# Kernel optimization log

Measured on AMD Instinct MI355X. Metric: run time of the kernel, lower is better.

Reference implementation:

```python
import jax, jax.numpy as jnp
import numpy as np

N_NODES = 100_000
N_EDGES = 3_200_000
IN_CH = 128
HID = 128


def setup_inputs() -> dict:
    key = jax.random.key(0)
    k1, k2, k3, k4, k5 = jax.random.split(key, 5)
    x = jax.random.normal(k1, (N_NODES, IN_CH), dtype=jnp.float32)
    edge_index = jax.random.randint(k2, (2, N_EDGES), 0, N_NODES, dtype=jnp.int64)
    # GCNConv params: glorot-style weights, zero bias (as in PyG defaults)
    s1 = 1.0 / np.sqrt(IN_CH)
    s2 = 1.0 / np.sqrt(HID)
    W1 = jax.random.uniform(k3, (IN_CH, HID), jnp.float32, -s1, s1)
    b1 = jnp.zeros((HID,), jnp.float32)
    W2 = jax.random.uniform(k4, (HID, HID), jnp.float32, -s2, s2)
    b2 = jnp.zeros((HID,), jnp.float32)
    return {"x": x, "edge_index": edge_index, "W1": W1, "b1": b1, "W2": W2, "b2": b2}


def _gcn_conv(x, src, dst, W, b):
    """PyG GCNConv: add self-loops, symmetric D^-1/2 (A+I) D^-1/2 norm,
    linear transform first, then aggregate, then bias."""
    n = x.shape[0]
    loops = jnp.arange(n, dtype=src.dtype)
    s = jnp.concatenate([src, loops])          # [E+N]
    d = jnp.concatenate([dst, loops])          # [E+N]
    w = jnp.ones(s.shape[0], dtype=x.dtype)    # edge_weight=None -> ones
    deg = jax.ops.segment_sum(w, d, num_segments=n)            # [N]
    dinv = jnp.where(deg > 0, jax.lax.rsqrt(deg), 0.0)         # deg^-1/2
    norm = dinv[s] * w * dinv[d]                                # [E+N]
    xw = x @ W                                                  # [N, H]
    msg = xw[s] * norm[:, None]                                 # [E+N, H] gather
    out = jax.ops.segment_sum(msg, d, num_segments=n)           # [N, H] scatter
    return out + b


def reference(x, edge_index, W1, b1, W2, b2):
    src, dst = edge_index[0], edge_index[1]
    h1 = jax.nn.relu(_gcn_conv(x, src, dst, W1, b1))
    h2 = jax.nn.relu(_gcn_conv(h1, src, dst, W2, b2))
    return jnp.concatenate([h1, h2], axis=1)   # [N, 2*HID]
```

## Files before the change

### kernel.cpp

```cpp
#include <hip/hip_runtime.h>
#include <hip/hip_bf16.h>
#include <stdint.h>

#define NN 100000
#define BSH 9
#define BSZ 512
#define NBUCK 196
#define CAP 24576

static __device__ __forceinline__ float bf_lo(unsigned int u) {
    union { unsigned int i; float f; } c; c.i = u << 16; return c.f;
}
static __device__ __forceinline__ float bf_hi(unsigned int u) {
    union { unsigned int i; float f; } c; c.i = u & 0xffff0000u; return c.f;
}
static __device__ __forceinline__ unsigned short f2bf(float f) {
    union { float f; unsigned int i; } c; c.f = f;
    unsigned int r = (c.i + 0x7fffu + ((c.i >> 16) & 1u)) >> 16;
    return (unsigned short)r;
}

__global__ void k_detect(const int* __restrict__ eb, int* __restrict__ flag) {
    int v = eb[2 * threadIdx.x + 1];
    unsigned long long m = __ballot(v == 0);
    if (threadIdx.x == 0) *flag = (m == ~0ull) ? 1 : 0;
}

__global__ void k_init(int* __restrict__ gcursor) {
    int i = threadIdx.x;
    if (i < NBUCK) gcursor[i] = i * CAP;
}

__global__ __launch_bounds__(256) void k_bucket(const int* __restrict__ eb, int E,
                                                const int* __restrict__ flag,
                                                int* __restrict__ gcursor,
                                                unsigned int* __restrict__ pairs) {
    __shared__ int hist[NBUCK];
    __shared__ int gbase[NBUCK];
    int t = threadIdx.x;
    int sh = *flag;
    size_t base = (size_t)blockIdx.x * 4096;
    for (int i = t; i < NBUCK; i += 256) hist[i] = 0;
    __syncthreads();
    int srcs[16], rank[16], bks[16], dls[16];
#pragma unroll
    for (int k = 0; k < 16; k++) {
        size_t e = base + (size_t)k * 256 + t;
        if (e < (size_t)E) {
            int s = eb[e << sh];
            int d = eb[((size_t)E + e) << sh];
            int b = d >> BSH;
            srcs[k] = s; bks[k] = b; dls[k] = d & (BSZ - 1);
            rank[k] = atomicAdd(&hist[b], 1);
        } else {
            bks[k] = -1;
        }
    }
    __syncthreads();
    for (int i = t; i < NBUCK; i += 256) {
        int c = hist[i];
        gbase[i] = (c > 0) ? atomicAdd(&gcursor[i], c) : 0;
    }
    __syncthreads();
#pragma unroll
    for (int k = 0; k < 16; k++) {
        if (bks[k] >= 0) {
            int pos = gbase[bks[k]] + rank[k];
            if (pos < (bks[k] + 1) * CAP)
                pairs[pos] = ((unsigned int)dls[k] << 17) | (unsigned int)srcs[k];
        }
    }
}

__global__ __launch_bounds__(256) void k_pass2(const unsigned int* __restrict__ pairs,
                                               const int* __restrict__ gcursor,
                                               int* __restrict__ csr, int* __restrict__ ptr,
                                               int* __restrict__ degv, float* __restrict__ dinv) {
    __shared__ int hist[BSZ];
    __shared__ int lofs[BSZ];
    __shared__ int cur[BSZ];
    __shared__ int scanw[256];
    __shared__ int lcsr[CAP];
    int b = blockIdx.x, t = threadIdx.x;
    int base = b * CAP;
    int cnt = gcursor[b] - base;
    if (cnt > CAP) cnt = CAP;
    for (int i = t; i < BSZ; i += 256) hist[i] = 0;
    __syncthreads();
    for (int i = t; i < cnt; i += 256) {
        unsigned int p = pairs[base + i];
        atomicAdd(&hist[p >> 17], 1);
    }
    __syncthreads();
    int a = hist[2 * t] + hist[2 * t + 1];
    scanw[t] = a;
    __syncthreads();
    for (int d = 1; d < 256; d <<= 1) {
        int x = (t >= d) ? scanw[t - d] : 0;
        __syncthreads();
        scanw[t] += x;
        __syncthreads();
    }
    int excl = scanw[t] - a;
    lofs[2 * t] = excl;
    lofs[2 * t + 1] = excl + hist[2 * t];
    cur[2 * t] = excl;
    cur[2 * t + 1] = excl + hist[2 * t];
    __syncthreads();
    for (int i = t; i < cnt; i += 256) {
        unsigned int p = pairs[base + i];
        int dl = p >> 17;
        int pos = atomicAdd(&cur[dl], 1);
        lcsr[pos] = (int)(p & 0x1FFFFu);
    }
    __syncthreads();
    for (int i = t; i < cnt; i += 256) csr[base + i] = lcsr[i];
    int n0 = b << BSH;
    for (int g = t; g < BSZ; g += 256) {
        int n = n0 + g;
        if (n < NN) {
            int dg = hist[g];
            degv[n] = dg;
            ptr[n] = base + lofs[g];
            dinv[n] = rsqrtf((float)(dg + 1));
        }
    }
}

__global__ __launch_bounds__(256) void k_gemm(const float* __restrict__ A, int lda,
                                              const float* __restrict__ W,
                                              unsigned short* __restrict__ outb, int M) {
    __shared__ float Wl[32 * 128];
    __shared__ float Al[64 * 33];
    int t = threadIdx.x;
    int row0 = blockIdx.x * 64;
    int cg = t & 15, rg = t >> 4;
    int c0 = cg * 8, r0 = rg * 4;
    float acc[4][8];
#pragma unroll
    for (int i = 0; i < 4; i++)
#pragma unroll
        for (int j = 0; j < 8; j++) acc[i][j] = 0.f;

    for (int kb = 0; kb < 4; kb++) {
        __syncthreads();
        const float4* Wg = (const float4*)(W + kb * 32 * 128);
        float4* Wl4 = (float4*)Wl;
#pragma unroll
        for (int i = 0; i < 4; i++) Wl4[t + 256 * i] = Wg[t + 256 * i];
#pragma unroll
        for (int i = 0; i < 2; i++) {
            int idx = t + 256 * i;
            int r = idx >> 3, c4 = idx & 7;
            int grow = row0 + r;
            float4 v = make_float4(0.f, 0.f, 0.f, 0.f);
            if (grow < M) v = *(const float4*)(A + (size_t)grow * lda + kb * 32 + c4 * 4);
            float* dp = &Al[r * 33 + c4 * 4];
            dp[0] = v.x; dp[1] = v.y; dp[2] = v.z; dp[3] = v.w;
        }
        __syncthreads();
#pragma unroll 8
        for (int k = 0; k < 32; k++) {
            float wv[8];
            *(float4*)&wv[0] = *(const float4*)&Wl[k * 128 + c0];
            *(float4*)&wv[4] = *(const float4*)&Wl[k * 128 + c0 + 4];
            float av[4];
#pragma unroll
            for (int i = 0; i < 4; i++) av[i] = Al[(r0 + i) * 33 + k];
#pragma unroll
            for (int i = 0; i < 4; i++)
#pragma unroll
                for (int j = 0; j < 8; j++)
                    acc[i][j] = fmaf(av[i], wv[j], acc[i][j]);
        }
    }
#pragma unroll
    for (int i = 0; i < 4; i++) {
        int grow = row0 + r0 + i;
        if (grow < M) {
            unsigned int w[4];
#pragma unroll
            for (int j = 0; j < 4; j++)
                w[j] = (unsigned int)f2bf(acc[i][2 * j]) | ((unsigned int)f2bf(acc[i][2 * j + 1]) << 16);
            uint4 pk = make_uint4(w[0], w[1], w[2], w[3]);
            *(uint4*)(outb + (size_t)grow * 128 + c0) = pk;
        }
    }
}

__global__ __launch_bounds__(256) void k_aggr(const unsigned short* __restrict__ xwb,
                                              const int* __restrict__ csr, const int* __restrict__ ptr,
                                              const int* __restrict__ degv,
                                              const float* __restrict__ dinv, const float* __restrict__ bias,
                                              float* __restrict__ outf, int N) {
    int wid = (blockIdx.x * 256 + threadIdx.x) >> 6;
    int lane = threadIdx.x & 63;
    if (wid >= N) return;
    int n = wid;
    int st = ptr[n];
    int en = st + degv[n];
    const unsigned short* xl = xwb + (lane << 1);
    float acc0 = 0.f, acc1 = 0.f;
    for (int j = st; j < en; j += 64) {
        int e = j + lane;
        int sp = (e < en) ? csr[e] : 0;
        float dp = (e < en) ? dinv[sp] : 0.f;
        int cnt = en - j; if (cnt > 64) cnt = 64;
        int cntr = (cnt + 3) & ~3;
        for (int q = 0; q < cntr; q += 4) {
            int s0 = __shfl(sp, q), s1 = __shfl(sp, q + 1);
            int s2 = __shfl(sp, q + 2), s3 = __shfl(sp, q + 3);
            float d0 = __shfl(dp, q), d1 = __shfl(dp, q + 1);
            float d2 = __shfl(dp, q + 2), d3 = __shfl(dp, q + 3);
            unsigned int u0 = *(const unsigned int*)(xl + ((size_t)s0 << 7));
            unsigned int u1 = *(const unsigned int*)(xl + ((size_t)s1 << 7));
            unsigned int u2 = *(const unsigned int*)(xl + ((size_t)s2 << 7));
            unsigned int u3 = *(const unsigned int*)(xl + ((size_t)s3 << 7));
            acc0 = fmaf(bf_lo(u0), d0, acc0); acc1 = fmaf(bf_hi(u0), d0, acc1);
            acc0 = fmaf(bf_lo(u1), d1, acc0); acc1 = fmaf(bf_hi(u1), d1, acc1);
            acc0 = fmaf(bf_lo(u2), d2, acc0); acc1 = fmaf(bf_hi(u2), d2, acc1);
            acc0 = fmaf(bf_lo(u3), d3, acc0); acc1 = fmaf(bf_hi(u3), d3, acc1);
        }
    }
    float dn = dinv[n];
    {
        unsigned int u = *(const unsigned int*)(xl + ((size_t)n << 7));
        acc0 = fmaf(bf_lo(u), dn, acc0);
        acc1 = fmaf(bf_hi(u), dn, acc1);
    }
    float o0 = fmaxf(fmaf(acc0, dn, bias[lane << 1]), 0.f);
    float o1 = fmaxf(fmaf(acc1, dn, bias[(lane << 1) + 1]), 0.f);
    *(float2*)(outf + (size_t)n * 256 + (lane << 1)) = make_float2(o0, o1);
}

extern "C" void kernel_launch(void* const* d_in, const int* in_sizes, int n_in,
                              void* d_out, int out_size, void* d_ws, size_t ws_size,
                              hipStream_t stream) {
    const float* x  = (const float*)d_in[0];
    const int*   eb = (const int*)d_in[1];
    const float* W1 = (const float*)d_in[2];
    const float* b1 = (const float*)d_in[3];
    const float* W2 = (const float*)d_in[4];
    const float* b2 = (const float*)d_in[5];
    float* out = (float*)d_out;

    int E = in_sizes[1] / 2;

    char* w = (char*)d_ws;
    size_t o = 0;
    auto carve = [&](size_t bytes) { char* p = w + o; o += (bytes + 255) & ~(size_t)255; return p; };
    int*   flag    = (int*)carve(4);
    int*   gcursor = (int*)carve((size_t)NBUCK * 4);
    int*   ptr     = (int*)carve((size_t)NN * 4);
    int*   deg     = (int*)carve((size_t)NN * 4);
    float* dinv    = (float*)carve((size_t)NN * 4);
    int*   csr     = (int*)carve((size_t)NBUCK * CAP * 4);
    size_t big = (size_t)NN * 128 * 2;
    size_t pb  = (size_t)NBUCK * CAP * 4;
    char* shared_region = carve(big > pb ? big : pb);
    unsigned int*   pairs = (unsigned int*)shared_region;
    unsigned short* xwb   = (unsigned short*)shared_region;
    (void)ws_size;

    int EB4 = (E + 4095) / 4096;
    int GB  = (NN + 63) / 64;
    int AB  = (NN + 3) / 4;

    k_detect<<<1, 64, 0, stream>>>(eb, flag);
    k_init<<<1, 256, 0, stream>>>(gcursor);
    k_bucket<<<EB4, 256, 0, stream>>>(eb, E, flag, gcursor, pairs);
    k_pass2<<<NBUCK, 256, 0, stream>>>(pairs, gcursor, csr, ptr, deg, dinv);

    k_gemm<<<GB, 256, 0, stream>>>(x, 128, W1, xwb, NN);
    k_aggr<<<AB, 256, 0, stream>>>(xwb, csr, ptr, deg, dinv, b1, out, NN);

    k_gemm<<<GB, 256, 0, stream>>>(out, 256, W2, xwb, NN);
    k_aggr<<<AB, 256, 0, stream>>>(xwb, csr, ptr, deg, dinv, b2, out + 128, NN);
}
```

Baseline: 538.4 us.

## Prescale GEMM output by dinv, sort neighbours by source, unroll gather by eight

The GEMM epilogue now multiplies each row by dinv[row] before the bf16 store. This removes the per-edge dinv gather and multiply from the aggregation loop, which becomes a plain sum unrolled by eight. Padding lanes point at a zeroed extra row NN that k_init clears. pass2 orders each node's neighbour list by the high bits of the source index to improve cache locality of the gathers. The separate detect kernel is folded into k_bucket. The costs are a larger shared-memory histogram in pass2, and bf16 rounding now happens after the dinv scaling.

```diff
diff --git a/kernel.cpp b/kernel.cpp
--- a/kernel.cpp
+++ b/kernel.cpp
@@ -20,28 +20,28 @@
     return (unsigned short)r;
 }
 
-__global__ void k_detect(const int* __restrict__ eb, int* __restrict__ flag) {
-    int v = eb[2 * threadIdx.x + 1];
-    unsigned long long m = __ballot(v == 0);
-    if (threadIdx.x == 0) *flag = (m == ~0ull) ? 1 : 0;
-}
-
-__global__ void k_init(int* __restrict__ gcursor) {
+__global__ void k_init(int* __restrict__ gcursor, unsigned int* __restrict__ xwb_row_nn) {
     int i = threadIdx.x;
     if (i < NBUCK) gcursor[i] = i * CAP;
+    if (i < 64) xwb_row_nn[i] = 0u;
 }
 
 __global__ __launch_bounds__(256) void k_bucket(const int* __restrict__ eb, int E,
-                                                const int* __restrict__ flag,
                                                 int* __restrict__ gcursor,
                                                 unsigned int* __restrict__ pairs) {
     __shared__ int hist[NBUCK];
     __shared__ int gbase[NBUCK];
+    __shared__ int shflag;
     int t = threadIdx.x;
-    int sh = *flag;
+    if (t < 64) {
+        int v = eb[2 * t + 1];
+        unsigned long long m = __ballot(v == 0);
+        if (t == 0) shflag = (m == ~0ull) ? 1 : 0;
+    }
+    for (int i = t; i < NBUCK; i += 256) hist[i] = 0;
+    __syncthreads();
+    int sh = shflag;
     size_t base = (size_t)blockIdx.x * 4096;
-    for (int i = t; i < NBUCK; i += 256) hist[i] = 0;
-    __syncthreads();
     int srcs[16], rank[16], bks[16], dls[16];
 #pragma unroll
     for (int k = 0; k < 16; k++) {
@@ -76,23 +76,30 @@
                                                const int* __restrict__ gcursor,
                                                int* __restrict__ csr, int* __restrict__ ptr,
                                                int* __restrict__ degv, float* __restrict__ dinv) {
+    __shared__ int hist2[BSZ * 8];
+    __shared__ int cur2[BSZ * 8];
     __shared__ int hist[BSZ];
     __shared__ int lofs[BSZ];
-    __shared__ int cur[BSZ];
     __shared__ int scanw[256];
     __shared__ int lcsr[CAP];
     int b = blockIdx.x, t = threadIdx.x;
     int base = b * CAP;
     int cnt = gcursor[b] - base;
     if (cnt > CAP) cnt = CAP;
-    for (int i = t; i < BSZ; i += 256) hist[i] = 0;
+    for (int i = t; i < BSZ * 8; i += 256) hist2[i] = 0;
     __syncthreads();
     for (int i = t; i < cnt; i += 256) {
         unsigned int p = pairs[base + i];
-        atomicAdd(&hist[p >> 17], 1);
-    }
-    __syncthreads();
-    int a = hist[2 * t] + hist[2 * t + 1];
+        int key = (int)((p >> 17) << 3) | (int)((p & 0x1FFFFu) >> 14);
+        atomicAdd(&hist2[key], 1);
+    }
+    __syncthreads();
+    int dl0 = 2 * t, dl1 = 2 * t + 1;
+    int h0 = 0, h1 = 0;
+#pragma unroll
+    for (int oc = 0; oc < 8; oc++) { h0 += hist2[(dl0 << 3) | oc]; h1 += hist2[(dl1 << 3) | oc]; }
+    hist[dl0] = h0; hist[dl1] = h1;
+    int a = h0 + h1;
     scanw[t] = a;
     __syncthreads();
     for (int d = 1; d < 256; d <<= 1) {
@@ -102,16 +109,20 @@
         __syncthreads();
     }
     int excl = scanw[t] - a;
-    lofs[2 * t] = excl;
-    lofs[2 * t + 1] = excl + hist[2 * t];
-    cur[2 * t] = excl;
-    cur[2 * t + 1] = excl + hist[2 * t];
+    lofs[dl0] = excl;
+    lofs[dl1] = excl + h0;
+    int run = excl;
+#pragma unroll
+    for (int oc = 0; oc < 8; oc++) { cur2[(dl0 << 3) | oc] = run; run += hist2[(dl0 << 3) | oc]; }
+#pragma unroll
+    for (int oc = 0; oc < 8; oc++) { cur2[(dl1 << 3) | oc] = run; run += hist2[(dl1 << 3) | oc]; }
     __syncthreads();
     for (int i = t; i < cnt; i += 256) {
         unsigned int p = pairs[base + i];
-        int dl = p >> 17;
-        int pos = atomicAdd(&cur[dl], 1);
-        lcsr[pos] = (int)(p & 0x1FFFFu);
+        int src = (int)(p & 0x1FFFFu);
+        int key = (int)((p >> 17) << 3) | (src >> 14);
+        int pos = atomicAdd(&cur2[key], 1);
+        lcsr[pos] = src;
     }
     __syncthreads();
     for (int i = t; i < cnt; i += 256) csr[base + i] = lcsr[i];
@@ -129,6 +140,7 @@
 
 __global__ __launch_bounds__(256) void k_gemm(const float* __restrict__ A, int lda,
                                               const float* __restrict__ W,
+                                              const float* __restrict__ dinv,
                                               unsigned short* __restrict__ outb, int M) {
     __shared__ float Wl[32 * 128];
     __shared__ float Al[64 * 33];
@@ -178,10 +190,12 @@
     for (int i = 0; i < 4; i++) {
         int grow = row0 + r0 + i;
         if (grow < M) {
+            float dv = dinv[grow];
             unsigned int w[4];
 #pragma unroll
             for (int j = 0; j < 4; j++)
-                w[j] = (unsigned int)f2bf(acc[i][2 * j]) | ((unsigned int)f2bf(acc[i][2 * j + 1]) << 16);
+                w[j] = (unsigned int)f2bf(acc[i][2 * j] * dv) |
+                       ((unsigned int)f2bf(acc[i][2 * j + 1] * dv) << 16);
             uint4 pk = make_uint4(w[0], w[1], w[2], w[3]);
             *(uint4*)(outb + (size_t)grow * 128 + c0) = pk;
         }
@@ -203,33 +217,41 @@
     float acc0 = 0.f, acc1 = 0.f;
     for (int j = st; j < en; j += 64) {
         int e = j + lane;
-        int sp = (e < en) ? csr[e] : 0;
-        float dp = (e < en) ? dinv[sp] : 0.f;
+        int sp = (e < en) ? csr[e] : NN;
         int cnt = en - j; if (cnt > 64) cnt = 64;
-        int cntr = (cnt + 3) & ~3;
-        for (int q = 0; q < cntr; q += 4) {
-            int s0 = __shfl(sp, q), s1 = __shfl(sp, q + 1);
+        int cntr = (cnt + 7) & ~7;
+        for (int q = 0; q < cntr; q += 8) {
+            int s0 = __shfl(sp, q),     s1 = __shfl(sp, q + 1);
             int s2 = __shfl(sp, q + 2), s3 = __shfl(sp, q + 3);
-            float d0 = __shfl(dp, q), d1 = __shfl(dp, q + 1);
-            float d2 = __shfl(dp, q + 2), d3 = __shfl(dp, q + 3);
+            int s4 = __shfl(sp, q + 4), s5 = __shfl(sp, q + 5);
+            int s6 = __shfl(sp, q + 6), s7 = __shfl(sp, q + 7);
             unsigned int u0 = *(const unsigned int*)(xl + ((size_t)s0 << 7));
             unsigned int u1 = *(const unsigned int*)(xl + ((size_t)s1 << 7));
             unsigned int u2 = *(const unsigned int*)(xl + ((size_t)s2 << 7));
             unsigned int u3 = *(const unsigned int*)(xl + ((size_t)s3 << 7));
-            acc0 = fmaf(bf_lo(u0), d0, acc0); acc1 = fmaf(bf_hi(u0), d0, acc1);
-            acc0 = fmaf(bf_lo(u1), d1, acc0); acc1 = fmaf(bf_hi(u1), d1, acc1);
-            acc0 = fmaf(bf_lo(u2), d2, acc0); acc1 = fmaf(bf_hi(u2), d2, acc1);
-            acc0 = fmaf(bf_lo(u3), d3, acc0); acc1 = fmaf(bf_hi(u3), d3, acc1);
-        }
-    }
-    float dn = dinv[n];
+            unsigned int u4 = *(const unsigned int*)(xl + ((size_t)s4 << 7));
+            unsigned int u5 = *(const unsigned int*)(xl + ((size_t)s5 << 7));
+            unsigned int u6 = *(const unsigned int*)(xl + ((size_t)s6 << 7));
+            unsigned int u7 = *(const unsigned int*)(xl + ((size_t)s7 << 7));
+            acc0 += bf_lo(u0); acc1 += bf_hi(u0);
+            acc0 += bf_lo(u1); acc1 += bf_hi(u1);
+            acc0 += bf_lo(u2); acc1 += bf_hi(u2);
+            acc0 += bf_lo(u3); acc1 += bf_hi(u3);
+            acc0 += bf_lo(u4); acc1 += bf_hi(u4);
+            acc0 += bf_lo(u5); acc1 += bf_hi(u5);
+            acc0 += bf_lo(u6); acc1 += bf_hi(u6);
+            acc0 += bf_lo(u7); acc1 += bf_hi(u7);
+        }
+    }
     {
         unsigned int u = *(const unsigned int*)(xl + ((size_t)n << 7));
-        acc0 = fmaf(bf_lo(u), dn, acc0);
-        acc1 = fmaf(bf_hi(u), dn, acc1);
-    }
-    float o0 = fmaxf(fmaf(acc0, dn, bias[lane << 1]), 0.f);
-    float o1 = fmaxf(fmaf(acc1, dn, bias[(lane << 1) + 1]), 0.f);
+        acc0 += bf_lo(u);
+        acc1 += bf_hi(u);
+    }
+    float dn = dinv[n];
+    float2 bv = *(const float2*)(bias + (lane << 1));
+    float o0 = fmaxf(fmaf(acc0, dn, bv.x), 0.f);
+    float o1 = fmaxf(fmaf(acc1, dn, bv.y), 0.f);
     *(float2*)(outf + (size_t)n * 256 + (lane << 1)) = make_float2(o0, o1);
 }
 
@@ -249,13 +271,12 @@
     char* w = (char*)d_ws;
     size_t o = 0;
     auto carve = [&](size_t bytes) { char* p = w + o; o += (bytes + 255) & ~(size_t)255; return p; };
-    int*   flag    = (int*)carve(4);
     int*   gcursor = (int*)carve((size_t)NBUCK * 4);
     int*   ptr     = (int*)carve((size_t)NN * 4);
     int*   deg     = (int*)carve((size_t)NN * 4);
     float* dinv    = (float*)carve((size_t)NN * 4);
     int*   csr     = (int*)carve((size_t)NBUCK * CAP * 4);
-    size_t big = (size_t)NN * 128 * 2;
+    size_t big = (size_t)(NN + 1) * 128 * 2;
     size_t pb  = (size_t)NBUCK * CAP * 4;
     char* shared_region = carve(big > pb ? big : pb);
     unsigned int*   pairs = (unsigned int*)shared_region;
@@ -266,14 +287,13 @@
     int GB  = (NN + 63) / 64;
     int AB  = (NN + 3) / 4;
 
-    k_detect<<<1, 64, 0, stream>>>(eb, flag);
-    k_init<<<1, 256, 0, stream>>>(gcursor);
-    k_bucket<<<EB4, 256, 0, stream>>>(eb, E, flag, gcursor, pairs);
+    k_init<<<1, 256, 0, stream>>>(gcursor, (unsigned int*)(xwb + (size_t)NN * 128));
+    k_bucket<<<EB4, 256, 0, stream>>>(eb, E, gcursor, pairs);
     k_pass2<<<NBUCK, 256, 0, stream>>>(pairs, gcursor, csr, ptr, deg, dinv);
 
-    k_gemm<<<GB, 256, 0, stream>>>(x, 128, W1, xwb, NN);
+    k_gemm<<<GB, 256, 0, stream>>>(x, 128, W1, dinv, xwb, NN);
     k_aggr<<<AB, 256, 0, stream>>>(xwb, csr, ptr, deg, dinv, b1, out, NN);
 
-    k_gemm<<<GB, 256, 0, stream>>>(out, 256, W2, xwb, NN);
+    k_gemm<<<GB, 256, 0, stream>>>(out, 256, W2, dinv, xwb, NN);
     k_aggr<<<AB, 256, 0, stream>>>(xwb, csr, ptr, deg, dinv, b2, out + 128, NN);
 }
```

Result: no change. 528.8 us (-1.8%).
